# Optimization experiments

Measured on AMD Instinct MI355X. Metric: run time of the kernel, lower is better.

Reference implementation:

```python
import jax, jax.numpy as jnp
import numpy as np

D_MODEL = 1024
NUM_HEADS = 16
HEAD_DIM = D_MODEL // NUM_HEADS


def setup_inputs() -> dict:
    key = jax.random.key(0)
    k1, k2, k3 = jax.random.split(key, 3)
    B, T = 4, 2048
    x = jax.random.normal(k1, (B, T, D_MODEL), dtype=jnp.float32)
    # nn.Linear weights: out = x @ W.T; store torch-layout [out_features, in_features]
    w_qkv = jax.random.normal(k2, (3 * D_MODEL, D_MODEL), dtype=jnp.float32) * (D_MODEL ** -0.5)
    w_proj = jax.random.normal(k3, (D_MODEL, D_MODEL), dtype=jnp.float32) * (D_MODEL ** -0.5)
    return {"x": x, "w_qkv": w_qkv, "w_proj": w_proj}


def reference(x, w_qkv, w_proj):
    B, T, C = x.shape
    H, Dh = NUM_HEADS, HEAD_DIM
    qkv = jnp.einsum('btc,fc->btf', x, w_qkv)          # [B,T,3C]
    q, k, v = jnp.split(qkv, 3, axis=2)
    # [B,T,C] -> [B,H,T,Dh]
    q = q.reshape(B, T, H, Dh).transpose(0, 2, 1, 3)
    k = k.reshape(B, T, H, Dh).transpose(0, 2, 1, 3)
    v = v.reshape(B, T, H, Dh).transpose(0, 2, 1, 3)
    scale = Dh ** -0.5
    att = jnp.einsum('bhqd,bhkd->bhqk', q, k) * scale  # [B,H,T,T]
    causal = jnp.tril(jnp.ones((T, T), dtype=bool))
    att = jnp.where(causal, att, -jnp.inf)
    att = jax.nn.softmax(att, axis=-1)
    y = jnp.einsum('bhqk,bhkd->bhqd', att, v)          # [B,H,T,Dh]
    y = y.transpose(0, 2, 1, 3).reshape(B, T, C)
    return jnp.einsum('btc,oc->bto', y, w_proj)
```

## Files before the change

kernel.cpp:

```cpp
#include <hip/hip_runtime.h>
#include <stdint.h>
#include <math.h>

typedef __bf16 bf16;
typedef __bf16 bf16x4 __attribute__((ext_vector_type(4)));
typedef __bf16 bf16x8 __attribute__((ext_vector_type(8)));
typedef float f32x4 __attribute__((ext_vector_type(4)));

#define MFMA16(a, b, c) __builtin_amdgcn_mfma_f32_16x16x32_bf16((a), (b), (c), 0, 0, 0)

typedef __attribute__((address_space(1))) void* as1v;
typedef __attribute__((address_space(3))) void* as3v;

__device__ __forceinline__ void async_ld16(const void* g, void* l) {
  __builtin_amdgcn_global_load_lds((as1v)(uintptr_t)g,
                                   (as3v)(unsigned int)(uintptr_t)l, 16, 0, 0);
}

__global__ __launch_bounds__(256) void cast3_k(const float* __restrict__ x,
                                               const float* __restrict__ wq,
                                               const float* __restrict__ wp,
                                               bf16* __restrict__ xb,
                                               bf16* __restrict__ wqb,
                                               bf16* __restrict__ wpb) {
  const long i = (long)blockIdx.x * 256 + threadIdx.x;
  const float4* src;
  bf16x4* dst;
  long off;
  if (i < 2097152L) {
    src = (const float4*)x;  dst = (bf16x4*)xb;  off = i;
  } else if (i < 2097152L + 786432L) {
    src = (const float4*)wq; dst = (bf16x4*)wqb; off = i - 2097152L;
  } else {
    src = (const float4*)wp; dst = (bf16x4*)wpb; off = i - 2097152L - 786432L;
  }
  float4 v = src[off];
  bf16x4 o;
  o[0] = (bf16)v.x; o[1] = (bf16)v.y; o[2] = (bf16)v.z; o[3] = (bf16)v.w;
  dst[off] = o;
}

__global__ __launch_bounds__(256, 2) void gemm_qkv(const bf16* __restrict__ A,
                                                   const bf16* __restrict__ Bm,
                                                   bf16* __restrict__ qb,
                                                   bf16* __restrict__ kb,
                                                   bf16* __restrict__ vth) {
  __shared__ bf16 As[2][128 * 64];
  __shared__ bf16 Bs[2][192 * 64];
  const int tid  = threadIdx.x;
  const int lane = tid & 63;
  const int wv   = tid >> 6;
  const int wm   = wv >> 1;
  const int wn   = wv & 1;
  const int lr   = lane & 15;
  const int quad = lane >> 4;
  const long m0 = (long)blockIdx.y * 128;
  const long n0 = (long)blockIdx.x * 192;

  const int srow = lane >> 3;
  const int scg  = (lane & 7) ^ srow;
  const int swz  = lr & 7;

  const f32x4 fz = {0.f, 0.f, 0.f, 0.f};
  f32x4 acc[4][6];
#pragma unroll
  for (int i = 0; i < 4; ++i)
#pragma unroll
    for (int j = 0; j < 6; ++j) acc[i][j] = fz;

#define STAGE_QKV(kt, bufi)                                                        \
  do {                                                                             \
    const long kk = (long)(kt) * 64;                                               \
    _Pragma("unroll") for (int i_ = 0; i_ < 4; ++i_)                               \
        async_ld16(&A[(m0 + i_ * 32 + wv * 8 + srow) * 1024 + kk + scg * 8],       \
                   &As[bufi][(i_ * 32 + wv * 8) * 64]);                            \
    _Pragma("unroll") for (int i_ = 0; i_ < 6; ++i_)                               \
        async_ld16(&Bm[(n0 + i_ * 32 + wv * 8 + srow) * 1024 + kk + scg * 8],      \
                   &Bs[bufi][(i_ * 32 + wv * 8) * 64]);                            \
  } while (0)

  STAGE_QKV(0, 0);

#pragma unroll 2
  for (int t = 0; t < 16; ++t) {
    const int cur = t & 1;
    if (t < 15) {
      STAGE_QKV(t + 1, cur ^ 1);
      asm volatile("s_waitcnt vmcnt(10)" ::: "memory");
    } else {
      asm volatile("s_waitcnt vmcnt(0)" ::: "memory");
    }
    __builtin_amdgcn_s_barrier();

    bf16x8 af[2][4], bfr[2][6];
#pragma unroll
    for (int ds = 0; ds < 2; ++ds) {
      const int slot = ((ds << 2) + quad) ^ swz;
#pragma unroll
      for (int mi = 0; mi < 4; ++mi)
        af[ds][mi] = *(const bf16x8*)&As[cur][(wm * 64 + mi * 16 + lr) * 64 + slot * 8];
#pragma unroll
      for (int ni = 0; ni < 6; ++ni)
        bfr[ds][ni] = *(const bf16x8*)&Bs[cur][(wn * 96 + ni * 16 + lr) * 64 + slot * 8];
    }
#pragma unroll
    for (int ds = 0; ds < 2; ++ds)
#pragma unroll
      for (int mi = 0; mi < 4; ++mi)
#pragma unroll
        for (int ni = 0; ni < 6; ++ni)
          acc[mi][ni] = MFMA16(af[ds][mi], bfr[ds][ni], acc[mi][ni]);

    if (t < 15) __builtin_amdgcn_s_barrier();
  }
#undef STAGE_QKV

  const float kS = 0.18033688f;
#pragma unroll
  for (int mi = 0; mi < 4; ++mi) {
    const long row = m0 + wm * 64 + mi * 16 + quad * 4;
#pragma unroll
    for (int ni = 0; ni < 6; ++ni) {
      const long col = n0 + wn * 96 + ni * 16 + lr;
      if (col < 1024) {
#pragma unroll
        for (int r = 0; r < 4; ++r) qb[(row + r) * 1024 + col] = (bf16)(acc[mi][ni][r] * kS);
      } else if (col < 2048) {
        const long kc = col - 1024;
#pragma unroll
        for (int r = 0; r < 4; ++r) kb[(row + r) * 1024 + kc] = (bf16)(acc[mi][ni][r]);
      } else {
        const long vcol = col - 2048;
        const long h = vcol >> 6, d = vcol & 63;
        const long b = row >> 11;
        const long tt = row & 2047;
        bf16x4 pk;
#pragma unroll
        for (int r = 0; r < 4; ++r) pk[r] = (bf16)(acc[mi][ni][r]);
        *(bf16x4*)&vth[(((b << 4) + h) * 64 + d) * 2048 + tt] = pk;
      }
    }
  }
}

__global__ __launch_bounds__(256, 2) void gemm_proj(const bf16* __restrict__ A,
                                                    const bf16* __restrict__ Bm,
                                                    float* __restrict__ C) {
  __shared__ bf16 As[2][128 * 64];
  __shared__ bf16 Bs[2][128 * 64];
  const int tid  = threadIdx.x;
  const int lane = tid & 63;
  const int wv   = tid >> 6;
  const int wm   = wv >> 1;
  const int wn   = wv & 1;
  const int lr   = lane & 15;
  const int quad = lane >> 4;
  const long m0 = (long)blockIdx.y * 128;
  const long n0 = (long)blockIdx.x * 128;

  const int srow = lane >> 3;
  const int scg  = (lane & 7) ^ srow;
  const int swz  = lr & 7;

  const f32x4 fz = {0.f, 0.f, 0.f, 0.f};
  f32x4 acc[4][4];
#pragma unroll
  for (int i = 0; i < 4; ++i)
#pragma unroll
    for (int j = 0; j < 4; ++j) acc[i][j] = fz;

#define STAGE_PROJ(kt, bufi)                                                       \
  do {                                                                             \
    const long kk = (long)(kt) * 64;                                               \
    _Pragma("unroll") for (int i_ = 0; i_ < 4; ++i_) {                             \
      const int rb = i_ * 32 + wv * 8;                                             \
      async_ld16(&A[(m0 + rb + srow) * 1024 + kk + scg * 8], &As[bufi][rb * 64]);  \
      async_ld16(&Bm[(n0 + rb + srow) * 1024 + kk + scg * 8], &Bs[bufi][rb * 64]); \
    }                                                                              \
  } while (0)

  STAGE_PROJ(0, 0);

#pragma unroll 2
  for (int t = 0; t < 16; ++t) {
    const int cur = t & 1;
    if (t < 15) {
      STAGE_PROJ(t + 1, cur ^ 1);
      asm volatile("s_waitcnt vmcnt(8)" ::: "memory");
    } else {
      asm volatile("s_waitcnt vmcnt(0)" ::: "memory");
    }
    __builtin_amdgcn_s_barrier();

    bf16x8 af[2][4], bfr[2][4];
#pragma unroll
    for (int ds = 0; ds < 2; ++ds) {
      const int slot = ((ds << 2) + quad) ^ swz;
#pragma unroll
      for (int mi = 0; mi < 4; ++mi)
        af[ds][mi] = *(const bf16x8*)&As[cur][(wm * 64 + mi * 16 + lr) * 64 + slot * 8];
#pragma unroll
      for (int ni = 0; ni < 4; ++ni)
        bfr[ds][ni] = *(const bf16x8*)&Bs[cur][(wn * 64 + ni * 16 + lr) * 64 + slot * 8];
    }
#pragma unroll
    for (int ds = 0; ds < 2; ++ds)
#pragma unroll
      for (int mi = 0; mi < 4; ++mi)
#pragma unroll
        for (int ni = 0; ni < 4; ++ni)
          acc[mi][ni] = MFMA16(af[ds][mi], bfr[ds][ni], acc[mi][ni]);

    if (t < 15) __builtin_amdgcn_s_barrier();
  }
#undef STAGE_PROJ

#pragma unroll
  for (int mi = 0; mi < 4; ++mi) {
    const long row = m0 + wm * 64 + mi * 16 + quad * 4;
#pragma unroll
    for (int ni = 0; ni < 4; ++ni) {
      const long col = n0 + wn * 64 + ni * 16 + lr;
#pragma unroll
      for (int r = 0; r < 4; ++r) C[(row + r) * 1024 + col] = acc[mi][ni][r];
    }
  }
}

__global__ __launch_bounds__(256, 2) void flash_attn5(const bf16* __restrict__ q,
                                                      const bf16* __restrict__ k,
                                                      const bf16* __restrict__ vth,
                                                      bf16* __restrict__ y) {
  __shared__ bf16 Ks[2][64 * 64];
  __shared__ bf16 Vt[64 * 64];
  __shared__ bf16 Ps[4][32 * 72];
  const int tid  = threadIdx.x;
  const int lane = tid & 63;
  const int wv   = tid >> 6;
  const int lr   = lane & 15;
  const int quad = lane >> 4;
  const int lin  = blockIdx.x + (blockIdx.y << 3);
  const int xcd  = lin & 7;
  const int slot = lin >> 3;
  const int p    = slot & 7;
  const int bh   = ((slot >> 3) << 3) | xcd;
  const int b = bh >> 4, h = bh & 15;
  const bf16* qp = q + ((size_t)b * 2048) * 1024 + h * 64;
  const bf16* kp = k + ((size_t)b * 2048) * 1024 + h * 64;
  const bf16* vp = vth + (size_t)bh * 64 * 2048;
  bf16* yp = y + ((size_t)b * 2048) * 1024 + h * 64;

  const int stg_row = lane >> 3;
  const int stg_cg  = (lane & 7) ^ stg_row;
  const int swz     = lr & 7;

  bf16x8 ones;
#pragma unroll
  for (int j = 0; j < 8; ++j) ones[j] = (bf16)1.0f;
  const f32x4 fz = {0.f, 0.f, 0.f, 0.f};

  for (int half = 0; half < 2; ++half) {
    const int qt = half ? p : 15 - p;
    const int q0 = qt * 128;
    const int kb_max = 2 * qt + 1;
    const int kmax_w = 2 * qt + (wv >> 1);

    bf16x8 qf[2][2];
#pragma unroll
    for (int nq = 0; nq < 2; ++nq) {
      const int qrow = q0 + wv * 32 + nq * 16 + lr;
#pragma unroll
      for (int ds = 0; ds < 2; ++ds)
        qf[nq][ds] = *(const bf16x8*)(qp + (size_t)qrow * 1024 + ds * 32 + quad * 8);
    }

    f32x4 o[2][4];
    f32x4 lacc[2];
#pragma unroll
    for (int nq = 0; nq < 2; ++nq) {
      lacc[nq] = fz;
#pragma unroll
      for (int nf = 0; nf < 4; ++nf) o[nq][nf] = fz;
    }

    __syncthreads();
#pragma unroll
    for (int i = 0; i < 2; ++i) {
      const int r = i * 32 + wv * 8 + stg_row;
      async_ld16(kp + (size_t)r * 1024 + stg_cg * 8, &Ks[0][(i * 32 + wv * 8) * 64]);
    }

    for (int kt = 0; kt <= kb_max; ++kt) {
      const int k0 = kt * 64;
      const int cb = kt & 1;
      __syncthreads();
      if (kt < kb_max) {
#pragma unroll
        for (int i = 0; i < 2; ++i) {
          const int r = i * 32 + wv * 8 + stg_row;
          async_ld16(kp + (size_t)(k0 + 64 + r) * 1024 + stg_cg * 8,
                     &Ks[cb ^ 1][(i * 32 + wv * 8) * 64]);
        }
      }
#pragma unroll
      for (int i = 0; i < 2; ++i) {
        const int r = i * 32 + wv * 8 + stg_row;
        async_ld16(vp + (size_t)r * 2048 + k0 + stg_cg * 8, &Vt[(i * 32 + wv * 8) * 64]);
      }

      const bool act = (kt <= kmax_w);
      bf16x8 ap[2][2];
      if (act) {
        f32x4 s[2][4];
#pragma unroll
        for (int nq = 0; nq < 2; ++nq)
#pragma unroll
          for (int mi = 0; mi < 4; ++mi) s[nq][mi] = fz;
#pragma unroll
        for (int ds = 0; ds < 2; ++ds)
#pragma unroll
          for (int mi = 0; mi < 4; ++mi) {
            const bf16x8 ak =
                *(const bf16x8*)&Ks[cb][(mi * 16 + lr) * 64 + (((ds << 2) + quad) ^ swz) * 8];
            s[0][mi] = MFMA16(ak, qf[0][ds], s[0][mi]);
            s[1][mi] = MFMA16(ak, qf[1][ds], s[1][mi]);
          }

        if (kt < kmax_w) {
#pragma unroll
          for (int nq = 0; nq < 2; ++nq) {
            const int qloc = nq * 16 + lr;
#pragma unroll
            for (int mi = 0; mi < 4; ++mi) {
              bf16x4 pb;
#pragma unroll
              for (int r = 0; r < 4; ++r) pb[r] = (bf16)__builtin_amdgcn_exp2f(s[nq][mi][r]);
              *(bf16x4*)&Ps[wv][qloc * 72 + mi * 16 + quad * 4] = pb;
            }
          }
        } else {
          const int kofs = k0 - q0 - wv * 32;
#pragma unroll
          for (int nq = 0; nq < 2; ++nq) {
            const int qloc = nq * 16 + lr;
#pragma unroll
            for (int mi = 0; mi < 4; ++mi) {
              bf16x4 pb;
#pragma unroll
              for (int r = 0; r < 4; ++r) {
                float pv = __builtin_amdgcn_exp2f(s[nq][mi][r]);
                if (mi * 16 + quad * 4 + r + kofs > qloc) pv = 0.0f;
                pb[r] = (bf16)pv;
              }
              *(bf16x4*)&Ps[wv][qloc * 72 + mi * 16 + quad * 4] = pb;
            }
          }
        }
#pragma unroll
        for (int ks = 0; ks < 2; ++ks) {
          ap[0][ks] = *(const bf16x8*)&Ps[wv][(lr) * 72 + ks * 32 + quad * 8];
          ap[1][ks] = *(const bf16x8*)&Ps[wv][(16 + lr) * 72 + ks * 32 + quad * 8];
        }
      }

      __syncthreads();

      if (act) {
#pragma unroll
        for (int ks = 0; ks < 2; ++ks) {
          lacc[0] = MFMA16(ap[0][ks], ones, lacc[0]);
          lacc[1] = MFMA16(ap[1][ks], ones, lacc[1]);
#pragma unroll
          for (int nf = 0; nf < 4; ++nf) {
            const bf16x8 bv =
                *(const bf16x8*)&Vt[(nf * 16 + lr) * 64 + (((ks << 2) + quad) ^ swz) * 8];
            o[0][nf] = MFMA16(ap[0][ks], bv, o[0][nf]);
            o[1][nf] = MFMA16(ap[1][ks], bv, o[1][nf]);
          }
        }
      }
    }

#pragma unroll
    for (int nq = 0; nq < 2; ++nq)
#pragma unroll
      for (int r = 0; r < 4; ++r) {
        const float inv = __builtin_amdgcn_rcpf(lacc[nq][r]);
        const int t = q0 + wv * 32 + nq * 16 + quad * 4 + r;
#pragma unroll
        for (int nf = 0; nf < 4; ++nf)
          yp[(size_t)t * 1024 + nf * 16 + lr] = (bf16)(o[nq][nf][r] * inv);
      }
  }
}

extern "C" void kernel_launch(void* const* d_in, const int* in_sizes, int n_in,
                              void* d_out, int out_size, void* d_ws, size_t ws_size,
                              hipStream_t stream) {
  const float* x      = (const float*)d_in[0];
  const float* w_qkv  = (const float*)d_in[1];
  const float* w_proj = (const float*)d_in[2];
  float* out = (float*)d_out;
  char* ws = (char*)d_ws;

  bf16* xb   = (bf16*)(ws);
  bf16* wqkb = (bf16*)(ws + (16ull << 20));
  bf16* wpb  = (bf16*)(ws + (22ull << 20));
  bf16* qb   = (bf16*)(ws + (24ull << 20));
  bf16* kbuf = (bf16*)(ws + (40ull << 20));
  bf16* vth  = (bf16*)(ws + (56ull << 20));
  bf16* yb   = (bf16*)(ws + (72ull << 20));

  cast3_k<<<dim3(12288), 256, 0, stream>>>(x, w_qkv, w_proj, xb, wqkb, wpb);
  gemm_qkv<<<dim3(16, 64), 256, 0, stream>>>(xb, wqkb, qb, kbuf, vth);
  flash_attn5<<<dim3(8, 64), 256, 0, stream>>>(qb, kbuf, vth, yb);
  gemm_proj<<<dim3(8, 64), 256, 0, stream>>>(yb, wpb, out);
}
```

Measured before the change: 216.6 us.

## Split QKV GEMM prefetch into two phases, add XCD block remap and setprio

The QKV projection GEMM now issues the next k-tile's global-to-LDS loads in two halves. A-tile plus the first B chunk go before the first half-k MFMA phase, and the remaining B chunks go after a mid-iteration barrier. This is meant to spread memory traffic across the compute and keep fewer loads outstanding per wait. It also remaps the block index so that consecutive M tiles land on the same XCD for L2 reuse, and raises wave priority around the MFMA bursts. The extra barrier per iteration and dropping the unroll-2 pragma may add sync overhead.

```diff
diff --git a/kernel.cpp b/kernel.cpp
--- a/kernel.cpp
+++ b/kernel.cpp
@@ -54,8 +54,12 @@
   const int wn   = wv & 1;
   const int lr   = lane & 15;
   const int quad = lane >> 4;
-  const long m0 = (long)blockIdx.y * 128;
-  const long n0 = (long)blockIdx.x * 192;
+
+  const int lin = blockIdx.x + (blockIdx.y << 4);
+  const int xcd = lin & 7;
+  const int idx = lin >> 3;
+  const long m0 = (long)(((idx >> 4) << 3) | xcd) * 128;
+  const long n0 = (long)(idx & 15) * 192;
 
   const int srow = lane >> 3;
   const int scg  = (lane & 7) ^ srow;
@@ -68,52 +72,77 @@
 #pragma unroll
     for (int j = 0; j < 6; ++j) acc[i][j] = fz;
 
-#define STAGE_QKV(kt, bufi)                                                        \
+#define STAGE_H1(kt, bufi)                                                         \
   do {                                                                             \
     const long kk = (long)(kt) * 64;                                               \
     _Pragma("unroll") for (int i_ = 0; i_ < 4; ++i_)                               \
         async_ld16(&A[(m0 + i_ * 32 + wv * 8 + srow) * 1024 + kk + scg * 8],       \
                    &As[bufi][(i_ * 32 + wv * 8) * 64]);                            \
-    _Pragma("unroll") for (int i_ = 0; i_ < 6; ++i_)                               \
+    async_ld16(&Bm[(n0 + wv * 8 + srow) * 1024 + kk + scg * 8],                    \
+               &Bs[bufi][(wv * 8) * 64]);                                          \
+  } while (0)
+#define STAGE_H2(kt, bufi)                                                         \
+  do {                                                                             \
+    const long kk = (long)(kt) * 64;                                               \
+    _Pragma("unroll") for (int i_ = 1; i_ < 6; ++i_)                               \
         async_ld16(&Bm[(n0 + i_ * 32 + wv * 8 + srow) * 1024 + kk + scg * 8],      \
                    &Bs[bufi][(i_ * 32 + wv * 8) * 64]);                            \
   } while (0)
 
-  STAGE_QKV(0, 0);
-
-#pragma unroll 2
+  STAGE_H1(0, 0);
+  STAGE_H2(0, 0);
+
   for (int t = 0; t < 16; ++t) {
     const int cur = t & 1;
     if (t < 15) {
-      STAGE_QKV(t + 1, cur ^ 1);
-      asm volatile("s_waitcnt vmcnt(10)" ::: "memory");
+      STAGE_H1(t + 1, cur ^ 1);
+      asm volatile("s_waitcnt vmcnt(5)" ::: "memory");
     } else {
       asm volatile("s_waitcnt vmcnt(0)" ::: "memory");
     }
     __builtin_amdgcn_s_barrier();
 
-    bf16x8 af[2][4], bfr[2][6];
-#pragma unroll
-    for (int ds = 0; ds < 2; ++ds) {
-      const int slot = ((ds << 2) + quad) ^ swz;
-#pragma unroll
-      for (int mi = 0; mi < 4; ++mi)
-        af[ds][mi] = *(const bf16x8*)&As[cur][(wm * 64 + mi * 16 + lr) * 64 + slot * 8];
+    {
+      const int slot = quad ^ swz;
+      bf16x8 af[4], bfr[6];
+#pragma unroll
+      for (int mi = 0; mi < 4; ++mi)
+        af[mi] = *(const bf16x8*)&As[cur][(wm * 64 + mi * 16 + lr) * 64 + slot * 8];
 #pragma unroll
       for (int ni = 0; ni < 6; ++ni)
-        bfr[ds][ni] = *(const bf16x8*)&Bs[cur][(wn * 96 + ni * 16 + lr) * 64 + slot * 8];
-    }
-#pragma unroll
-    for (int ds = 0; ds < 2; ++ds)
+        bfr[ni] = *(const bf16x8*)&Bs[cur][(wn * 96 + ni * 16 + lr) * 64 + slot * 8];
+      __builtin_amdgcn_s_setprio(1);
 #pragma unroll
       for (int mi = 0; mi < 4; ++mi)
 #pragma unroll
         for (int ni = 0; ni < 6; ++ni)
-          acc[mi][ni] = MFMA16(af[ds][mi], bfr[ds][ni], acc[mi][ni]);
-
+          acc[mi][ni] = MFMA16(af[mi], bfr[ni], acc[mi][ni]);
+      __builtin_amdgcn_s_setprio(0);
+    }
+    __builtin_amdgcn_s_barrier();
+
+    if (t < 15) STAGE_H2(t + 1, cur ^ 1);
+    {
+      const int slot = (4 + quad) ^ swz;
+      bf16x8 af[4], bfr[6];
+#pragma unroll
+      for (int mi = 0; mi < 4; ++mi)
+        af[mi] = *(const bf16x8*)&As[cur][(wm * 64 + mi * 16 + lr) * 64 + slot * 8];
+#pragma unroll
+      for (int ni = 0; ni < 6; ++ni)
+        bfr[ni] = *(const bf16x8*)&Bs[cur][(wn * 96 + ni * 16 + lr) * 64 + slot * 8];
+      __builtin_amdgcn_s_setprio(1);
+#pragma unroll
+      for (int mi = 0; mi < 4; ++mi)
+#pragma unroll
+        for (int ni = 0; ni < 6; ++ni)
+          acc[mi][ni] = MFMA16(af[mi], bfr[ni], acc[mi][ni]);
+      __builtin_amdgcn_s_setprio(0);
+    }
     if (t < 15) __builtin_amdgcn_s_barrier();
   }
-#undef STAGE_QKV
+#undef STAGE_H1
+#undef STAGE_H2
 
   const float kS = 0.18033688f;
 #pragma unroll
```

Result: slower. 224.1 us (+3.5%).
